# Kernel optimization log

Hardware: AMD Instinct MI355X
Metric: run time of the kernel (lower is better)

Reference implementation:

```python
import jax, jax.numpy as jnp
import numpy as np

D_MODEL = 1024
NUM_HEADS = 16
D_K = D_MODEL // NUM_HEADS


def setup_inputs() -> dict:
    key = jax.random.key(0)
    ks = jax.random.split(key, 12)
    B, S, D = 2, 2048, D_MODEL
    s = 1.0 / np.sqrt(D)
    inp = {
        "Q": jax.random.normal(ks[0], (B, S, D), jnp.float32),
        "K": jax.random.normal(ks[1], (B, S, D), jnp.float32),
        "V": jax.random.normal(ks[2], (B, S, D), jnp.float32),
        "Wq": jax.random.normal(ks[3], (D, D), jnp.float32) * s,
        "bq": jax.random.normal(ks[4], (D,), jnp.float32) * s,
        "Wk": jax.random.normal(ks[5], (D, D), jnp.float32) * s,
        "bk": jax.random.normal(ks[6], (D,), jnp.float32) * s,
        "Wv": jax.random.normal(ks[7], (D, D), jnp.float32) * s,
        "bv": jax.random.normal(ks[8], (D,), jnp.float32) * s,
        "Wo": jax.random.normal(ks[9], (D, D), jnp.float32) * s,
        "bo": jax.random.normal(ks[10], (D,), jnp.float32) * s,
    }
    return inp


def _split_heads(x, B, S):
    # [B, S, D] -> [B, H, S, d_k]
    return x.reshape(B, S, NUM_HEADS, D_K).transpose(0, 2, 1, 3)


def reference(Q, K, V, Wq, bq, Wk, bk, Wv, bv, Wo, bo):
    B, S, D = Q.shape
    # torch nn.Linear: y = x @ W.T + b
    q = _split_heads(Q @ Wq.T + bq, B, S)
    k = _split_heads(K @ Wk.T + bk, B, S)
    v = _split_heads(V @ Wv.T + bv, B, S)
    scale = 1.0 / np.sqrt(D_K).astype(np.float32)
    # [B, H, S, S] attention scores (materialized, as in the original)
    scores = jnp.einsum('bhqd,bhkd->bhqk', q, k) * scale
    probs = jax.nn.softmax(scores, axis=-1)
    out = jnp.einsum('bhqk,bhkd->bhqd', probs, v)
    out = out.transpose(0, 2, 1, 3).reshape(B, S, D)
    return out @ Wo.T + bo
```

## Files before the change

kernel.cpp:

```cpp
#include <hip/hip_runtime.h>
#include <hip/hip_bf16.h>

#define S_LEN   2048
#define NHEADS  16
#define DKH     64
#define DMODEL  1024
#define NBATCH  2

typedef __bf16 bf16x8 __attribute__((ext_vector_type(8)));
typedef __bf16 bf16x4 __attribute__((ext_vector_type(4)));
typedef float  f32x4  __attribute__((ext_vector_type(4)));

typedef __attribute__((address_space(3))) void       lds_void;
typedef const __attribute__((address_space(1))) void glob_void;

__device__ __forceinline__ void glds16(const void* g, void* l) {
    __builtin_amdgcn_global_load_lds((glob_void*)g, (lds_void*)l, 16, 0, 0);
}

struct CvtArgs {
    const float* src[7];
    __bf16*      dst[7];
    int          n[7];
};

__global__ __launch_bounds__(256)
void cvt_all_k(CvtArgs a)
{
    const int t = blockIdx.y;
    const size_t i = ((size_t)blockIdx.x * 256 + threadIdx.x) * 8;
    if ((int)i >= a.n[t]) return;
    const float* s = a.src[t];
    f32x4 lo = *(const f32x4*)(s + i);
    f32x4 hi = *(const f32x4*)(s + i + 4);
    bf16x8 r;
#pragma unroll
    for (int k = 0; k < 4; ++k) { r[k] = (__bf16)lo[k]; r[4 + k] = (__bf16)hi[k]; }
    *(bf16x8*)(a.dst[t] + i) = r;
}

__device__ __forceinline__ void gemm_core(
    const __bf16* __restrict__ A, const __bf16* __restrict__ W,
    int m0, int n0, int K,
    __bf16 (*As)[64], __bf16 (*Ws)[64], f32x4 acc[4][4])
{
    const int tid  = threadIdx.x;
    const int lane = tid & 63;
    const int wv   = tid >> 6;
    const int l15  = lane & 15;
    const int quad = lane >> 4;
    const int wm   = wv >> 1;
    const int wn   = wv & 1;
    const int srow = lane >> 3;
    const int scol = ((lane & 7) ^ srow) << 3;

    const __bf16* ag[4]; const __bf16* wg[4];
    void* al[4]; void* wl[4];
#pragma unroll
    for (int i = 0; i < 4; ++i) {
        const int r = wv * 8 + i * 32 + srow;
        ag[i] = A + (size_t)(m0 + r) * K + scol;
        wg[i] = W + (size_t)(n0 + r) * K + scol;
        al[i] = &As[wv * 8 + i * 32][0];
        wl[i] = &Ws[wv * 8 + i * 32][0];
    }

    for (int k0 = 0;;) {
        __syncthreads();
#pragma unroll
        for (int i = 0; i < 4; ++i) { glds16(ag[i] + k0, al[i]); glds16(wg[i] + k0, wl[i]); }
        __syncthreads();

#pragma unroll
        for (int kh = 0; kh < 2; ++kh) {
            bf16x8 af[4], wf[4];
#pragma unroll
            for (int i = 0; i < 4; ++i) {
                const int row = wm * 64 + i * 16 + l15;
                af[i] = *(const bf16x8*)((const char*)&As[row][0]
                        + (((quad << 4) + (kh << 6)) ^ ((row & 7) << 4)));
            }
#pragma unroll
            for (int j = 0; j < 4; ++j) {
                const int row = wn * 64 + j * 16 + l15;
                wf[j] = *(const bf16x8*)((const char*)&Ws[row][0]
                        + (((quad << 4) + (kh << 6)) ^ ((row & 7) << 4)));
            }
#pragma unroll
            for (int i = 0; i < 4; ++i)
#pragma unroll
                for (int j = 0; j < 4; ++j)
                    acc[i][j] = __builtin_amdgcn_mfma_f32_16x16x32_bf16(af[i], wf[j], acc[i][j], 0, 0, 0);
        }
        k0 += 64;
        if (k0 >= K) break;
    }
}

struct GArgs {
    const __bf16* A[3];
    const __bf16* W[3];
    const float*  bias[3];
    __bf16*       out[3];
};

__global__ __launch_bounds__(256)
void gemm_qkv(GArgs g, int z_off)
{
    __shared__ __align__(16) __bf16 As[128][64];
    __shared__ __align__(16) __bf16 Ws[128][64];

    const int fid = blockIdx.x;
    const int z   = (fid >> 8) + z_off;
    const int f8  = fid & 255;
    int m0, n0;
    if (z == 2) { m0 = (f8 & 7) * 128;  n0 = (f8 >> 3) * 128; }
    else        { m0 = (f8 & 31) * 128; n0 = (f8 >> 5) * 128; }

    f32x4 acc[4][4];
#pragma unroll
    for (int i = 0; i < 4; ++i)
#pragma unroll
        for (int j = 0; j < 4; ++j) acc[i][j] = (f32x4){0.f, 0.f, 0.f, 0.f};

    gemm_core(g.A[z], g.W[z], m0, n0, DMODEL, As, Ws, acc);

    const int lane = threadIdx.x & 63;
    const int wv   = threadIdx.x >> 6;
    const int l15  = lane & 15;
    const int quad = lane >> 4;
    const int wm   = wv >> 1;
    const int wn   = wv & 1;
    const float* bias = g.bias[z];
    __bf16* out = g.out[z];
    const float oscale = (z == 0) ? 0.125f * 1.44269504088896f : 1.0f;

#pragma unroll
    for (int j = 0; j < 4; ++j) {
        const int col = n0 + wn * 64 + j * 16 + l15;
        const float bcol = (z == 2) ? 0.f : bias[col];
#pragma unroll
        for (int i = 0; i < 4; ++i) {
#pragma unroll
            for (int r = 0; r < 4; ++r) {
                const int row = m0 + wm * 64 + i * 16 + quad * 4 + r;
                size_t idx;
                float v = acc[i][j][r];
                if (z == 2) {
                    const int h = row >> 6, d = row & (DKH - 1);
                    const int b = col >> 11, s = col & (S_LEN - 1);
                    v += bias[row];
                    idx = ((size_t)(b * NHEADS + h) * DKH + d) * S_LEN + s;
                } else {
                    const int b = row >> 11, s = row & (S_LEN - 1);
                    const int h = col >> 6, d = col & (DKH - 1);
                    v = (v + bcol) * oscale;
                    idx = ((size_t)(b * NHEADS + h) * S_LEN + s) * DKH + d;
                }
                out[idx] = (__bf16)v;
            }
        }
    }
}

__global__ __launch_bounds__(256)
void gemm_out(const __bf16* __restrict__ A, const __bf16* __restrict__ W,
              const float* __restrict__ bias, float* __restrict__ out)
{
    __shared__ __align__(16) __bf16 As[128][64];
    __shared__ __align__(16) __bf16 Ws[128][64];

    const int fid = blockIdx.x;
    const int m0 = (fid & 31) * 128;
    const int n0 = (fid >> 5) * 128;

    f32x4 acc[4][4];
#pragma unroll
    for (int i = 0; i < 4; ++i)
#pragma unroll
        for (int j = 0; j < 4; ++j) acc[i][j] = (f32x4){0.f, 0.f, 0.f, 0.f};

    gemm_core(A, W, m0, n0, DMODEL, As, Ws, acc);

    const int lane = threadIdx.x & 63;
    const int wv   = threadIdx.x >> 6;
    const int l15  = lane & 15;
    const int quad = lane >> 4;
    const int wm   = wv >> 1;
    const int wn   = wv & 1;

#pragma unroll
    for (int j = 0; j < 4; ++j) {
        const int col = n0 + wn * 64 + j * 16 + l15;
        const float bv = bias[col];
#pragma unroll
        for (int i = 0; i < 4; ++i)
#pragma unroll
            for (int r = 0; r < 4; ++r) {
                const int row = m0 + wm * 64 + i * 16 + quad * 4 + r;
                out[(size_t)row * DMODEL + col] = acc[i][j][r] + bv;
            }
    }
}

__global__ __launch_bounds__(256, 2)
void attn_k(const __bf16* __restrict__ Qh, const __bf16* __restrict__ Kh,
            const __bf16* __restrict__ VhT, __bf16* __restrict__ out,
            float* __restrict__ opart, float* __restrict__ lpart, int ksplit)
{
    __shared__ __align__(16) __bf16 Ks[128][72];
    __shared__ __align__(16) __bf16 Vs[64][136];

    const int tid  = threadIdx.x;
    const int lane = tid & 63;
    const int wv   = tid >> 6;
    const int l15  = lane & 15;
    const int quad = lane >> 4;

    const int fid  = blockIdx.x;
    const int x    = fid & 7;
    const int j    = fid >> 3;
    const int bh   = x * 4 + (j & 3);
    const int rest = j >> 2;
    const int q0   = (rest & 15) * 128;
    const int kh   = rest >> 4;
    const int klen = S_LEN / ksplit;
    const int kbeg = kh * klen;
    const int b  = bh >> 4;
    const int h  = bh & (NHEADS - 1);

    const __bf16* Q  = Qh  + (size_t)bh * S_LEN * DKH;
    const __bf16* Kp = Kh  + (size_t)bh * S_LEN * DKH;
    const __bf16* Vt = VhT + (size_t)bh * DKH * S_LEN;

    const int qrA = q0 + wv * 32 + l15;
    const int qrB = qrA + 16;
    const bf16x8 qa0 = *(const bf16x8*)(Q + (size_t)qrA * DKH + quad * 8);
    const bf16x8 qa1 = *(const bf16x8*)(Q + (size_t)qrA * DKH + quad * 8 + 32);
    const bf16x8 qb0 = *(const bf16x8*)(Q + (size_t)qrB * DKH + quad * 8);
    const bf16x8 qb1 = *(const bf16x8*)(Q + (size_t)qrB * DKH + quad * 8 + 32);

    const int krow = tid >> 1;
    const int kc0  = (tid & 1) * 32;
    const int vrow = tid >> 2;
    const int vc0  = (tid & 3) * 32;
    const __bf16* kst = Kp + (size_t)krow * DKH   + kc0;
    const __bf16* vst = Vt + (size_t)vrow * S_LEN + vc0;

    f32x4 oA[4], oB[4];
#pragma unroll
    for (int jj = 0; jj < 4; ++jj) {
        oA[jj] = (f32x4){0.f, 0.f, 0.f, 0.f};
        oB[jj] = (f32x4){0.f, 0.f, 0.f, 0.f};
    }
    float laccA = 0.f, laccB = 0.f;

    bf16x8 kr[4], vr[4];
#pragma unroll
    for (int i = 0; i < 4; ++i) kr[i] = *(const bf16x8*)(kst + (size_t)kbeg * DKH + 8 * i);
#pragma unroll
    for (int i = 0; i < 4; ++i) vr[i] = *(const bf16x8*)(vst + kbeg + 8 * i);

    for (int kt = kbeg; kt < kbeg + klen; kt += 128) {
        __syncthreads();
#pragma unroll
        for (int i = 0; i < 4; ++i) *(bf16x8*)&Ks[krow][kc0 + 8 * i] = kr[i];
#pragma unroll
        for (int i = 0; i < 4; ++i) *(bf16x8*)&Vs[vrow][vc0 + 8 * i] = vr[i];
        __syncthreads();
        if (kt + 128 < kbeg + klen) {
#pragma unroll
            for (int i = 0; i < 4; ++i)
                kr[i] = *(const bf16x8*)(kst + (size_t)(kt + 128) * DKH + 8 * i);
#pragma unroll
            for (int i = 0; i < 4; ++i)
                vr[i] = *(const bf16x8*)(vst + (kt + 128) + 8 * i);
        }

#pragma unroll
        for (int ht = 0; ht < 2; ++ht) {
            __builtin_amdgcn_s_setprio(1);
            float pA[4][4], pB[4][4];
#pragma unroll
            for (int n = 0; n < 4; ++n) {
                bf16x8 kA = *(const bf16x8*)&Ks[ht * 64 + n * 16 + l15][quad * 8];
                bf16x8 kB = *(const bf16x8*)&Ks[ht * 64 + n * 16 + l15][quad * 8 + 32];
                f32x4 sA = {0.f, 0.f, 0.f, 0.f};
                f32x4 sB = {0.f, 0.f, 0.f, 0.f};
                sA = __builtin_amdgcn_mfma_f32_16x16x32_bf16(kA, qa0, sA, 0, 0, 0);
                sB = __builtin_amdgcn_mfma_f32_16x16x32_bf16(kA, qb0, sB, 0, 0, 0);
                sA = __builtin_amdgcn_mfma_f32_16x16x32_bf16(kB, qa1, sA, 0, 0, 0);
                sB = __builtin_amdgcn_mfma_f32_16x16x32_bf16(kB, qb1, sB, 0, 0, 0);
#pragma unroll
                for (int r = 0; r < 4; ++r) {
                    pA[n][r] = __builtin_amdgcn_exp2f(sA[r]);
                    pB[n][r] = __builtin_amdgcn_exp2f(sB[r]);
                }
            }
#pragma unroll
            for (int n = 0; n < 4; ++n)
#pragma unroll
                for (int r = 0; r < 4; ++r) { laccA += pA[n][r]; laccB += pB[n][r]; }

#pragma unroll
            for (int t = 0; t < 2; ++t) {
                bf16x8 pfA, pfB;
#pragma unroll
                for (int jj = 0; jj < 4; ++jj) {
                    pfA[jj]     = (__bf16)pA[2 * t][jj];
                    pfA[4 + jj] = (__bf16)pA[2 * t + 1][jj];
                    pfB[jj]     = (__bf16)pB[2 * t][jj];
                    pfB[4 + jj] = (__bf16)pB[2 * t + 1][jj];
                }
#pragma unroll
                for (int jt = 0; jt < 4; ++jt) {
                    bf16x4 v0 = *(const bf16x4*)&Vs[jt * 16 + l15][ht * 64 + t * 32 + quad * 4];
                    bf16x4 v1 = *(const bf16x4*)&Vs[jt * 16 + l15][ht * 64 + t * 32 + 16 + quad * 4];
                    bf16x8 vf;
#pragma unroll
                    for (int jj = 0; jj < 4; ++jj) { vf[jj] = v0[jj]; vf[4 + jj] = v1[jj]; }
                    oA[jt] = __builtin_amdgcn_mfma_f32_16x16x32_bf16(vf, pfA, oA[jt], 0, 0, 0);
                    oB[jt] = __builtin_amdgcn_mfma_f32_16x16x32_bf16(vf, pfB, oB[jt], 0, 0, 0);
                }
            }
            __builtin_amdgcn_s_setprio(0);
        }
    }

    laccA += __shfl_xor(laccA, 16);
    laccA += __shfl_xor(laccA, 32);
    laccB += __shfl_xor(laccB, 16);
    laccB += __shfl_xor(laccB, 32);

    if (ksplit == 1) {
        const float invA = 1.0f / laccA;
        const float invB = 1.0f / laccB;
        __bf16* opA = out + ((size_t)b * S_LEN + qrA) * DMODEL + h * DKH;
        __bf16* opB = out + ((size_t)b * S_LEN + qrB) * DMODEL + h * DKH;
#pragma unroll
        for (int jt = 0; jt < 4; ++jt) {
            bf16x4 tA, tB;
#pragma unroll
            for (int r = 0; r < 4; ++r) {
                tA[r] = (__bf16)(oA[jt][r] * invA);
                tB[r] = (__bf16)(oB[jt][r] * invB);
            }
            *(bf16x4*)(opA + jt * 16 + quad * 4) = tA;
            *(bf16x4*)(opB + jt * 16 + quad * 4) = tB;
        }
    } else {
        float* pa = opart + ((size_t)(kh * 32 + bh) * S_LEN + qrA) * DKH;
        float* pb = opart + ((size_t)(kh * 32 + bh) * S_LEN + qrB) * DKH;
#pragma unroll
        for (int jt = 0; jt < 4; ++jt) {
            *(f32x4*)(pa + jt * 16 + quad * 4) = oA[jt];
            *(f32x4*)(pb + jt * 16 + quad * 4) = oB[jt];
        }
        if (quad == 0) {
            lpart[(size_t)(kh * 32 + bh) * S_LEN + qrA] = laccA;
            lpart[(size_t)(kh * 32 + bh) * S_LEN + qrB] = laccB;
        }
    }
}

__global__ __launch_bounds__(256)
void attn_combine(const float* __restrict__ opart, const float* __restrict__ lpart,
                  __bf16* __restrict__ out)
{
    const int t  = blockIdx.x * 256 + threadIdx.x;
    const int d8 = t & 7;
    const int s  = (t >> 3) & (S_LEN - 1);
    const int bh = t >> 14;
    const size_t half = (size_t)32 * S_LEN * DKH;
    const size_t base = ((size_t)bh * S_LEN + s) * DKH + d8 * 8;
    f32x4 a0 = *(const f32x4*)(opart + base);
    f32x4 a1 = *(const f32x4*)(opart + base + 4);
    f32x4 b0 = *(const f32x4*)(opart + base + half);
    f32x4 b1 = *(const f32x4*)(opart + base + half + 4);
    const float inv = 1.0f / (lpart[(size_t)bh * S_LEN + s]
                            + lpart[(size_t)(32 + bh) * S_LEN + s]);
    bf16x8 r;
#pragma unroll
    for (int k = 0; k < 4; ++k) {
        r[k]     = (__bf16)((a0[k] + b0[k]) * inv);
        r[4 + k] = (__bf16)((a1[k] + b1[k]) * inv);
    }
    const int bb = bh >> 4, hh = bh & (NHEADS - 1);
    *(bf16x8*)(out + ((size_t)bb * S_LEN + s) * DMODEL + hh * DKH + d8 * 8) = r;
}

extern "C" void kernel_launch(void* const* d_in, const int* in_sizes, int n_in,
                              void* d_out, int out_size, void* d_ws, size_t ws_size,
                              hipStream_t stream) {
    const float* Qi = (const float*)d_in[0];
    const float* Ki = (const float*)d_in[1];
    const float* Vi = (const float*)d_in[2];
    const float* Wq = (const float*)d_in[3];
    const float* bq = (const float*)d_in[4];
    const float* Wk = (const float*)d_in[5];
    const float* bk = (const float*)d_in[6];
    const float* Wv = (const float*)d_in[7];
    const float* bv = (const float*)d_in[8];
    const float* Wo = (const float*)d_in[9];
    const float* bo = (const float*)d_in[10];
    float* out = (float*)d_out;

    const int M = NBATCH * S_LEN;
    const size_t NW = (size_t)DMODEL * DMODEL;
    const size_t NE = (size_t)M * DMODEL;
    const size_t MB = (size_t)1 << 20;

    __bf16* w_bf   = (__bf16*)d_ws;
    __bf16* q_ws   = w_bf + 4 * NW;
    __bf16* k_ws   = q_ws + NE;
    __bf16* vT_big = k_ws + NE;
    __bf16* Qin_bf = vT_big + NE;
    __bf16* Kin_bf = Qin_bf + NE;
    __bf16* Vin_bf = Kin_bf + NE;
    float*  opart  = (float*)Qin_bf;
    float*  lpart  = (float*)((char*)d_ws + 64 * MB);
    __bf16* attn2  = (__bf16*)((char*)d_ws + 65 * MB);

    const bool big   = ws_size >= 56 * MB;
    const int ksplit = (ws_size >= 73 * MB) ? 2 : 1;
    __bf16* vT_ws   = big ? vT_big : Kin_bf;
    __bf16* attn_ws = (ksplit == 2) ? attn2 : Qin_bf;
    __bf16* wq_bf = w_bf, *wk_bf = w_bf + NW, *wv_bf = w_bf + 2 * NW, *wo_bf = w_bf + 3 * NW;

    CvtArgs ca;
    ca.src[0] = Wq; ca.src[1] = Wk; ca.src[2] = Wv; ca.src[3] = Wo;
    ca.src[4] = Qi; ca.src[5] = Ki; ca.src[6] = Vi;
    ca.dst[0] = wq_bf; ca.dst[1] = wk_bf; ca.dst[2] = wv_bf; ca.dst[3] = wo_bf;
    ca.dst[4] = Qin_bf; ca.dst[5] = Kin_bf; ca.dst[6] = Vin_bf;
    for (int t = 0; t < 4; ++t) ca.n[t] = (int)NW;
    for (int t = 4; t < 7; ++t) ca.n[t] = (int)NE;
    cvt_all_k<<<dim3(2048, 7), 256, 0, stream>>>(ca);

    GArgs g;
    g.A[0] = Qin_bf; g.W[0] = wq_bf; g.bias[0] = bq; g.out[0] = q_ws;
    g.A[1] = Kin_bf; g.W[1] = wk_bf; g.bias[1] = bk; g.out[1] = k_ws;
    g.A[2] = wv_bf;  g.W[2] = Vin_bf; g.bias[2] = bv; g.out[2] = vT_ws;
    if (big) {
        gemm_qkv<<<dim3(768), 256, 0, stream>>>(g, 0);
    } else {
        gemm_qkv<<<dim3(512), 256, 0, stream>>>(g, 0);
        gemm_qkv<<<dim3(256), 256, 0, stream>>>(g, 2);
    }

    attn_k<<<dim3(512 * ksplit), dim3(256), 0, stream>>>(q_ws, k_ws, vT_ws, attn_ws,
                                                         opart, lpart, ksplit);
    if (ksplit == 2)
        attn_combine<<<dim3(2048), 256, 0, stream>>>(opart, lpart, attn_ws);

    gemm_out<<<dim3(256), 256, 0, stream>>>(attn_ws, wo_bf, bo, out);
}
```

Baseline: 233.4 us.

## Enlarge attention Q tile, double-buffer K via direct-to-LDS loads, shrink GEMM K-step

The attention kernel now gives each wave 64 query rows instead of 32 and each block 256 rows, which halves the grid and reuses every K/V fragment read from LDS across four query sub-tiles. K tiles are loaded with global_load_lds into a swizzled double buffer instead of going through registers. Separately, the GEMM core drops from a 64-wide swizzled K-step to a 32-wide unswizzled step with half the LDS. The larger attention tile raises register pressure and may lower occupancy; the GEMM change doubles the barrier count per K and may bring LDS bank conflicts back.

```diff
diff --git a/kernel.cpp b/kernel.cpp
--- a/kernel.cpp
+++ b/kernel.cpp
@@ -42,7 +42,7 @@
 __device__ __forceinline__ void gemm_core(
     const __bf16* __restrict__ A, const __bf16* __restrict__ W,
     int m0, int n0, int K,
-    __bf16 (*As)[64], __bf16 (*Ws)[64], f32x4 acc[4][4])
+    __bf16 (*As)[32], __bf16 (*Ws)[32], f32x4 acc[4][4])
 {
     const int tid  = threadIdx.x;
     const int lane = tid & 63;
@@ -51,48 +51,40 @@
     const int quad = lane >> 4;
     const int wm   = wv >> 1;
     const int wn   = wv & 1;
-    const int srow = lane >> 3;
-    const int scol = ((lane & 7) ^ srow) << 3;
-
-    const __bf16* ag[4]; const __bf16* wg[4];
-    void* al[4]; void* wl[4];
-#pragma unroll
-    for (int i = 0; i < 4; ++i) {
-        const int r = wv * 8 + i * 32 + srow;
-        ag[i] = A + (size_t)(m0 + r) * K + scol;
-        wg[i] = W + (size_t)(n0 + r) * K + scol;
-        al[i] = &As[wv * 8 + i * 32][0];
-        wl[i] = &Ws[wv * 8 + i * 32][0];
-    }
+    const int grow = lane >> 2;
+    const int gcol = (lane & 3) * 8;
+
+    const __bf16* ag0 = A + (size_t)(m0 + wv * 32 + grow) * K + gcol;
+    const __bf16* ag1 = A + (size_t)(m0 + wv * 32 + 16 + grow) * K + gcol;
+    const __bf16* wg0 = W + (size_t)(n0 + wv * 32 + grow) * K + gcol;
+    const __bf16* wg1 = W + (size_t)(n0 + wv * 32 + 16 + grow) * K + gcol;
+    void* al0 = &As[wv * 32][0];
+    void* al1 = &As[wv * 32 + 16][0];
+    void* wl0 = &Ws[wv * 32][0];
+    void* wl1 = &Ws[wv * 32 + 16][0];
 
     for (int k0 = 0;;) {
         __syncthreads();
-#pragma unroll
-        for (int i = 0; i < 4; ++i) { glds16(ag[i] + k0, al[i]); glds16(wg[i] + k0, wl[i]); }
+        glds16(ag0 + k0, al0);
+        glds16(ag1 + k0, al1);
+        glds16(wg0 + k0, wl0);
+        glds16(wg1 + k0, wl1);
         __syncthreads();
 
-#pragma unroll
-        for (int kh = 0; kh < 2; ++kh) {
-            bf16x8 af[4], wf[4];
-#pragma unroll
-            for (int i = 0; i < 4; ++i) {
-                const int row = wm * 64 + i * 16 + l15;
-                af[i] = *(const bf16x8*)((const char*)&As[row][0]
-                        + (((quad << 4) + (kh << 6)) ^ ((row & 7) << 4)));
-            }
-#pragma unroll
-            for (int j = 0; j < 4; ++j) {
-                const int row = wn * 64 + j * 16 + l15;
-                wf[j] = *(const bf16x8*)((const char*)&Ws[row][0]
-                        + (((quad << 4) + (kh << 6)) ^ ((row & 7) << 4)));
-            }
-#pragma unroll
-            for (int i = 0; i < 4; ++i)
-#pragma unroll
-                for (int j = 0; j < 4; ++j)
-                    acc[i][j] = __builtin_amdgcn_mfma_f32_16x16x32_bf16(af[i], wf[j], acc[i][j], 0, 0, 0);
-        }
-        k0 += 64;
+        bf16x8 af[4], wf[4];
+#pragma unroll
+        for (int i = 0; i < 4; ++i)
+            af[i] = *(const bf16x8*)&As[wm * 64 + i * 16 + l15][quad * 8];
+#pragma unroll
+        for (int j = 0; j < 4; ++j)
+            wf[j] = *(const bf16x8*)&Ws[wn * 64 + j * 16 + l15][quad * 8];
+#pragma unroll
+        for (int i = 0; i < 4; ++i)
+#pragma unroll
+            for (int j = 0; j < 4; ++j)
+                acc[i][j] = __builtin_amdgcn_mfma_f32_16x16x32_bf16(af[i], wf[j], acc[i][j], 0, 0, 0);
+
+        k0 += 32;
         if (k0 >= K) break;
     }
 }
@@ -107,8 +99,8 @@
 __global__ __launch_bounds__(256)
 void gemm_qkv(GArgs g, int z_off)
 {
-    __shared__ __align__(16) __bf16 As[128][64];
-    __shared__ __align__(16) __bf16 Ws[128][64];
+    __shared__ __align__(16) __bf16 As[128][32];
+    __shared__ __align__(16) __bf16 Ws[128][32];
 
     const int fid = blockIdx.x;
     const int z   = (fid >> 8) + z_off;
@@ -167,8 +159,8 @@
 void gemm_out(const __bf16* __restrict__ A, const __bf16* __restrict__ W,
               const float* __restrict__ bias, float* __restrict__ out)
 {
-    __shared__ __align__(16) __bf16 As[128][64];
-    __shared__ __align__(16) __bf16 Ws[128][64];
+    __shared__ __align__(16) __bf16 As[128][32];
+    __shared__ __align__(16) __bf16 Ws[128][32];
 
     const int fid = blockIdx.x;
     const int m0 = (fid & 31) * 128;
@@ -208,7 +200,7 @@
             const __bf16* __restrict__ VhT, __bf16* __restrict__ out,
             float* __restrict__ opart, float* __restrict__ lpart, int ksplit)
 {
-    __shared__ __align__(16) __bf16 Ks[128][72];
+    __shared__ __align__(16) __bf16 Ks[2][128][64];
     __shared__ __align__(16) __bf16 Vs[64][136];
 
     const int tid  = threadIdx.x;
@@ -222,8 +214,8 @@
     const int j    = fid >> 3;
     const int bh   = x * 4 + (j & 3);
     const int rest = j >> 2;
-    const int q0   = (rest & 15) * 128;
-    const int kh   = rest >> 4;
+    const int q0   = (rest & 7) * 256;
+    const int kh   = rest >> 3;
     const int klen = S_LEN / ksplit;
     const int kbeg = kh * klen;
     const int b  = bh >> 4;
@@ -233,45 +225,53 @@
     const __bf16* Kp = Kh  + (size_t)bh * S_LEN * DKH;
     const __bf16* Vt = VhT + (size_t)bh * DKH * S_LEN;
 
-    const int qrA = q0 + wv * 32 + l15;
-    const int qrB = qrA + 16;
-    const bf16x8 qa0 = *(const bf16x8*)(Q + (size_t)qrA * DKH + quad * 8);
-    const bf16x8 qa1 = *(const bf16x8*)(Q + (size_t)qrA * DKH + quad * 8 + 32);
-    const bf16x8 qb0 = *(const bf16x8*)(Q + (size_t)qrB * DKH + quad * 8);
-    const bf16x8 qb1 = *(const bf16x8*)(Q + (size_t)qrB * DKH + quad * 8 + 32);
-
-    const int krow = tid >> 1;
-    const int kc0  = (tid & 1) * 32;
+    const int qr0 = q0 + wv * 64 + l15;
+    bf16x8 qf[4][2];
+#pragma unroll
+    for (int s = 0; s < 4; ++s) {
+        qf[s][0] = *(const bf16x8*)(Q + (size_t)(qr0 + s * 16) * DKH + quad * 8);
+        qf[s][1] = *(const bf16x8*)(Q + (size_t)(qr0 + s * 16) * DKH + quad * 8 + 32);
+    }
+
+    const int srow = lane >> 3;
+    const int scol = ((lane & 7) ^ srow) << 3;
+    char* const ksbase = (char*)&Ks[0][0][0];
+    const __bf16* kg[4];
+    int kdst[4];
+#pragma unroll
+    for (int i = 0; i < 4; ++i) {
+        const int r = wv * 8 + i * 32 + srow;
+        kg[i]   = Kp + (size_t)r * DKH + scol;
+        kdst[i] = (wv * 8 + i * 32) * 128;
+    }
+
     const int vrow = tid >> 2;
     const int vc0  = (tid & 3) * 32;
-    const __bf16* kst = Kp + (size_t)krow * DKH   + kc0;
     const __bf16* vst = Vt + (size_t)vrow * S_LEN + vc0;
 
-    f32x4 oA[4], oB[4];
-#pragma unroll
-    for (int jj = 0; jj < 4; ++jj) {
-        oA[jj] = (f32x4){0.f, 0.f, 0.f, 0.f};
-        oB[jj] = (f32x4){0.f, 0.f, 0.f, 0.f};
-    }
-    float laccA = 0.f, laccB = 0.f;
-
-    bf16x8 kr[4], vr[4];
-#pragma unroll
-    for (int i = 0; i < 4; ++i) kr[i] = *(const bf16x8*)(kst + (size_t)kbeg * DKH + 8 * i);
+    f32x4 o[4][4];
+#pragma unroll
+    for (int s = 0; s < 4; ++s)
+#pragma unroll
+        for (int jt = 0; jt < 4; ++jt) o[s][jt] = (f32x4){0.f, 0.f, 0.f, 0.f};
+    float lacc[4] = {0.f, 0.f, 0.f, 0.f};
+
+    int koff = 0;
+#pragma unroll
+    for (int i = 0; i < 4; ++i) glds16(kg[i] + (size_t)kbeg * DKH, ksbase + kdst[i]);
+    bf16x8 vr[4];
 #pragma unroll
     for (int i = 0; i < 4; ++i) vr[i] = *(const bf16x8*)(vst + kbeg + 8 * i);
 
     for (int kt = kbeg; kt < kbeg + klen; kt += 128) {
         __syncthreads();
-#pragma unroll
-        for (int i = 0; i < 4; ++i) *(bf16x8*)&Ks[krow][kc0 + 8 * i] = kr[i];
 #pragma unroll
         for (int i = 0; i < 4; ++i) *(bf16x8*)&Vs[vrow][vc0 + 8 * i] = vr[i];
         __syncthreads();
         if (kt + 128 < kbeg + klen) {
 #pragma unroll
             for (int i = 0; i < 4; ++i)
-                kr[i] = *(const bf16x8*)(kst + (size_t)(kt + 128) * DKH + 8 * i);
+                glds16(kg[i] + (size_t)(kt + 128) * DKH, ksbase + (koff ^ 16384) + kdst[i]);
 #pragma unroll
             for (int i = 0; i < 4; ++i)
                 vr[i] = *(const bf16x8*)(vst + (kt + 128) + 8 * i);
@@ -280,38 +280,51 @@
 #pragma unroll
         for (int ht = 0; ht < 2; ++ht) {
             __builtin_amdgcn_s_setprio(1);
-            float pA[4][4], pB[4][4];
-#pragma unroll
-            for (int n = 0; n < 4; ++n) {
-                bf16x8 kA = *(const bf16x8*)&Ks[ht * 64 + n * 16 + l15][quad * 8];
-                bf16x8 kB = *(const bf16x8*)&Ks[ht * 64 + n * 16 + l15][quad * 8 + 32];
-                f32x4 sA = {0.f, 0.f, 0.f, 0.f};
-                f32x4 sB = {0.f, 0.f, 0.f, 0.f};
-                sA = __builtin_amdgcn_mfma_f32_16x16x32_bf16(kA, qa0, sA, 0, 0, 0);
-                sB = __builtin_amdgcn_mfma_f32_16x16x32_bf16(kA, qb0, sB, 0, 0, 0);
-                sA = __builtin_amdgcn_mfma_f32_16x16x32_bf16(kB, qa1, sA, 0, 0, 0);
-                sB = __builtin_amdgcn_mfma_f32_16x16x32_bf16(kB, qb1, sB, 0, 0, 0);
-#pragma unroll
-                for (int r = 0; r < 4; ++r) {
-                    pA[n][r] = __builtin_amdgcn_exp2f(sA[r]);
-                    pB[n][r] = __builtin_amdgcn_exp2f(sB[r]);
+            bf16x8 pf[4][2];
+#pragma unroll
+            for (int tp = 0; tp < 2; ++tp) {
+                float p[4][2][4];
+#pragma unroll
+                for (int ni = 0; ni < 2; ++ni) {
+                    const int row = ht * 64 + (tp * 2 + ni) * 16 + l15;
+                    const char* kb = ksbase + koff + row * 128;
+                    const int sw = (row & 7) << 4;
+                    bf16x8 kA = *(const bf16x8*)(kb + ((quad << 4) ^ sw));
+                    bf16x8 kB = *(const bf16x8*)(kb + (((quad << 4) + 64) ^ sw));
+                    f32x4 s0 = {0.f, 0.f, 0.f, 0.f};
+                    f32x4 s1 = {0.f, 0.f, 0.f, 0.f};
+                    f32x4 s2 = {0.f, 0.f, 0.f, 0.f};
+                    f32x4 s3 = {0.f, 0.f, 0.f, 0.f};
+                    s0 = __builtin_amdgcn_mfma_f32_16x16x32_bf16(kA, qf[0][0], s0, 0, 0, 0);
+                    s1 = __builtin_amdgcn_mfma_f32_16x16x32_bf16(kA, qf[1][0], s1, 0, 0, 0);
+                    s2 = __builtin_amdgcn_mfma_f32_16x16x32_bf16(kA, qf[2][0], s2, 0, 0, 0);
+                    s3 = __builtin_amdgcn_mfma_f32_16x16x32_bf16(kA, qf[3][0], s3, 0, 0, 0);
+                    s0 = __builtin_amdgcn_mfma_f32_16x16x32_bf16(kB, qf[0][1], s0, 0, 0, 0);
+                    s1 = __builtin_amdgcn_mfma_f32_16x16x32_bf16(kB, qf[1][1], s1, 0, 0, 0);
+                    s2 = __builtin_amdgcn_mfma_f32_16x16x32_bf16(kB, qf[2][1], s2, 0, 0, 0);
+                    s3 = __builtin_amdgcn_mfma_f32_16x16x32_bf16(kB, qf[3][1], s3, 0, 0, 0);
+#pragma unroll
+                    for (int r = 0; r < 4; ++r) {
+                        p[0][ni][r] = __builtin_amdgcn_exp2f(s0[r]);
+                        p[1][ni][r] = __builtin_amdgcn_exp2f(s1[r]);
+                        p[2][ni][r] = __builtin_amdgcn_exp2f(s2[r]);
+                        p[3][ni][r] = __builtin_amdgcn_exp2f(s3[r]);
+                    }
+                }
+#pragma unroll
+                for (int s = 0; s < 4; ++s) {
+#pragma unroll
+                    for (int r = 0; r < 4; ++r) lacc[s] += p[s][0][r] + p[s][1][r];
+#pragma unroll
+                    for (int jj = 0; jj < 4; ++jj) {
+                        pf[s][tp][jj]     = (__bf16)p[s][0][jj];
+                        pf[s][tp][4 + jj] = (__bf16)p[s][1][jj];
+                    }
                 }
             }
-#pragma unroll
-            for (int n = 0; n < 4; ++n)
-#pragma unroll
-                for (int r = 0; r < 4; ++r) { laccA += pA[n][r]; laccB += pB[n][r]; }
 
 #pragma unroll
             for (int t = 0; t < 2; ++t) {
-                bf16x8 pfA, pfB;
-#pragma unroll
-                for (int jj = 0; jj < 4; ++jj) {
-                    pfA[jj]     = (__bf16)pA[2 * t][jj];
-                    pfA[4 + jj] = (__bf16)pA[2 * t + 1][jj];
-                    pfB[jj]     = (__bf16)pB[2 * t][jj];
-                    pfB[4 + jj] = (__bf16)pB[2 * t + 1][jj];
-                }
 #pragma unroll
                 for (int jt = 0; jt < 4; ++jt) {
                     bf16x4 v0 = *(const bf16x4*)&Vs[jt * 16 + l15][ht * 64 + t * 32 + quad * 4];
@@ -319,46 +332,45 @@
                     bf16x8 vf;
 #pragma unroll
                     for (int jj = 0; jj < 4; ++jj) { vf[jj] = v0[jj]; vf[4 + jj] = v1[jj]; }
-                    oA[jt] = __builtin_amdgcn_mfma_f32_16x16x32_bf16(vf, pfA, oA[jt], 0, 0, 0);
-                    oB[jt] = __builtin_amdgcn_mfma_f32_16x16x32_bf16(vf, pfB, oB[jt], 0, 0, 0);
+                    o[0][jt] = __builtin_amdgcn_mfma_f32_16x16x32_bf16(vf, pf[0][t], o[0][jt], 0, 0, 0);
+                    o[1][jt] = __builtin_amdgcn_mfma_f32_16x16x32_bf16(vf, pf[1][t], o[1][jt], 0, 0, 0);
+                    o[2][jt] = __builtin_amdgcn_mfma_f32_16x16x32_bf16(vf, pf[2][t], o[2][jt], 0, 0, 0);
+                    o[3][jt] = __builtin_amdgcn_mfma_f32_16x16x32_bf16(vf, pf[3][t], o[3][jt], 0, 0, 0);
                 }
             }
             __builtin_amdgcn_s_setprio(0);
         }
-    }
-
-    laccA += __shfl_xor(laccA, 16);
-    laccA += __shfl_xor(laccA, 32);
-    laccB += __shfl_xor(laccB, 16);
-    laccB += __shfl_xor(laccB, 32);
+        koff ^= 16384;
+    }
+
+#pragma unroll
+    for (int s = 0; s < 4; ++s) {
+        lacc[s] += __shfl_xor(lacc[s], 16);
+        lacc[s] += __shfl_xor(lacc[s], 32);
+    }
 
     if (ksplit == 1) {
-        const float invA = 1.0f / laccA;
-        const float invB = 1.0f / laccB;
-        __bf16* opA = out + ((size_t)b * S_LEN + qrA) * DMODEL + h * DKH;
-        __bf16* opB = out + ((size_t)b * S_LEN + qrB) * DMODEL + h * DKH;
-#pragma unroll
-        for (int jt = 0; jt < 4; ++jt) {
-            bf16x4 tA, tB;
-#pragma unroll
-            for (int r = 0; r < 4; ++r) {
-                tA[r] = (__bf16)(oA[jt][r] * invA);
-                tB[r] = (__bf16)(oB[jt][r] * invB);
+#pragma unroll
+        for (int s = 0; s < 4; ++s) {
+            const float inv = 1.0f / lacc[s];
+            __bf16* op = out + ((size_t)b * S_LEN + qr0 + s * 16) * DMODEL + h * DKH;
+#pragma unroll
+            for (int jt = 0; jt < 4; ++jt) {
+                bf16x4 tb;
+#pragma unroll
+                for (int r = 0; r < 4; ++r) tb[r] = (__bf16)(o[s][jt][r] * inv);
+                *(bf16x4*)(op + jt * 16 + quad * 4) = tb;
             }
-            *(bf16x4*)(opA + jt * 16 + quad * 4) = tA;
-            *(bf16x4*)(opB + jt * 16 + quad * 4) = tB;
         }
     } else {
-        float* pa = opart + ((size_t)(kh * 32 + bh) * S_LEN + qrA) * DKH;
-        float* pb = opart + ((size_t)(kh * 32 + bh) * S_LEN + qrB) * DKH;
-#pragma unroll
-        for (int jt = 0; jt < 4; ++jt) {
-            *(f32x4*)(pa + jt * 16 + quad * 4) = oA[jt];
-            *(f32x4*)(pb + jt * 16 + quad * 4) = oB[jt];
-        }
-        if (quad == 0) {
-            lpart[(size_t)(kh * 32 + bh) * S_LEN + qrA] = laccA;
-            lpart[(size_t)(kh * 32 + bh) * S_LEN + qrB] = laccB;
+#pragma unroll
+        for (int s = 0; s < 4; ++s) {
+            float* pa = opart + ((size_t)(kh * 32 + bh) * S_LEN + qr0 + s * 16) * DKH;
+#pragma unroll
+            for (int jt = 0; jt < 4; ++jt)
+                *(f32x4*)(pa + jt * 16 + quad * 4) = o[s][jt];
+            if (quad == 0)
+                lpart[(size_t)(kh * 32 + bh) * S_LEN + qr0 + s * 16] = lacc[s];
         }
     }
 }
@@ -447,7 +459,7 @@
         gemm_qkv<<<dim3(256), 256, 0, stream>>>(g, 2);
     }
 
-    attn_k<<<dim3(512 * ksplit), dim3(256), 0, stream>>>(q_ws, k_ws, vT_ws, attn_ws,
+    attn_k<<<dim3(256 * ksplit), dim3(256), 0, stream>>>(q_ws, k_ws, vT_ws, attn_ws,
                                                          opart, lpart, ksplit);
     if (ksplit == 2)
         attn_combine<<<dim3(2048), 256, 0, stream>>>(opart, lpart, attn_ws);
```

Result: no change. 230.8 us (-1.1%).
